# Kernel optimization log

Measured on AMD Instinct MI355X. Metric: run time of the kernel, lower is better.

The kernel has to match this reference:

```python
import jax, jax.numpy as jnp
import numpy as np

ORDER = 25
L = ORDER + 1
K = 64
B = 262144
N_ITER = 8
WEIGHT_FLOOR = 1e-05
VAR_FLOOR = 1e-06
LOG_PI = L * float(np.log(2.0 * np.pi))  # (order+1)*log(2*pi)


def setup_inputs() -> dict:
    key = jax.random.key(0)
    k1, k2 = jax.random.split(key)
    x = jax.random.normal(k1, (B, L), dtype=jnp.float32)
    mu0 = jax.random.normal(k2, (K, L), dtype=jnp.float32)      # torch.randn(K, L)
    w0 = jnp.ones((K,), dtype=jnp.float32)                      # normalized to 1/K in reference
    sigma0 = jnp.ones((K, L), dtype=jnp.float32)                # diagonal of eye(L)
    return {"x": x, "w0": w0, "mu0": mu0, "sigma0": sigma0}


def _em_step(x, w, mu, sig):
    # ---- E-step (diag covariance path of the torch module) ----
    log_det = jnp.sum(jnp.log(sig), axis=-1)                    # [K]
    prec = 1.0 / sig                                            # [K,L]
    # mahala[b,k] = sum_l (x[b,l]-mu[k,l])^2 * prec[k,l]
    # expanded quadratic form to avoid materializing [B,K,L]
    mahala = ((x * x) @ prec.T
              - 2.0 * (x @ (mu * prec).T)
              + jnp.sum(mu * mu * prec, axis=-1))               # [B,K]
    numer = jnp.log(w) - 0.5 * (LOG_PI + log_det + mahala)      # [B,K]
    denom = jax.scipy.special.logsumexp(numer, axis=-1, keepdims=True)
    posterior = jnp.exp(numer - denom)                          # [B,K]
    ll = jnp.sum(denom)
    # ---- M-step (alpha == 0) ----
    z = jnp.sum(posterior, axis=0)                              # [K]
    w_new = z / B
    zinv = 1.0 / z
    # weight flooring + renormalization
    w_new = jnp.maximum(w_new, WEIGHT_FLOOR)
    sum_floor = WEIGHT_FLOOR * K
    a = (1.0 - sum_floor) / (jnp.sum(w_new) - sum_floor)
    b = WEIGHT_FLOOR * (1.0 - a)
    w_new = a * w_new + b
    px = posterior.T @ x                                        # [K,L]
    mu_new = px * zinv[:, None]
    pxx = posterior.T @ (x * x)                                 # [K,L]
    sig_new = pxx * zinv[:, None] - mu_new * mu_new
    sig_new = jnp.maximum(sig_new, VAR_FLOOR)                   # variance flooring
    return w_new, mu_new, sig_new, ll


def reference(x, w0, mu0, sigma0):
    w = w0 / jnp.sum(w0)                                        # == 1/K for ones init

    def body(carry, _):
        w, mu, sig, _ = carry
        w, mu, sig, ll = _em_step(x, w, mu, sig)
        return (w, mu, sig, ll), None

    init = (w, mu0, sigma0, jnp.zeros((), dtype=jnp.float32))
    (w, mu, sig, ll), _ = jax.lax.scan(body, init, None, length=N_ITER)
    sigma = jax.vmap(jnp.diag)(sig)                             # [K,L,L] diagonal covariances
    return w, mu, sigma, ll
```

## Files before the change

kernel.cpp:

```cpp
#include <hip/hip_runtime.h>
#include <math.h>

typedef _Float16 f16x8 __attribute__((ext_vector_type(8)));
typedef float f32x16 __attribute__((ext_vector_type(16)));
typedef unsigned int uint4v __attribute__((ext_vector_type(4)));

namespace {
constexpr int LDIM = 26;
constexpr int KDIM = 64;
constexpr int NSAMP = 262144;
constexpr int NITER = 8;
constexpr float WFLOOR = 1e-5f;
constexpr float VFLOOR = 1e-6f;
constexpr float LOG2PI_TERM = 47.784803726642976f;
constexpr float L2E = 1.44269504088896340736f;
constexpr float LN2 = 0.69314718055994530942f;

constexpr int ACC_STRIDE = 53;
constexpr int ACC_N = KDIM * ACC_STRIDE + 1;
constexpr int NCOPIES = 8;
constexpr int WROW = 36;
constexpr int NBLK = 2048;
constexpr int PART_STRIDE = 3408;
}

__device__ float g_partial[NBLK * PART_STRIDE];
__device__ float g_accum[NCOPIES * ACC_N];
__device__ float g_w[KDIM];
__device__ float g_mu[KDIM * LDIM];
__device__ float g_sig[KDIM * LDIM];
__device__ float g_ll[1];
__device__ __align__(16) unsigned g_coef[KDIM * WROW];

__device__ __forceinline__ unsigned pkrtz(float a, float b) {
  return __builtin_bit_cast(unsigned, __builtin_amdgcn_cvt_pkrtz(a, b));
}
__device__ __forceinline__ f16x8 ld8h(const unsigned* p) {
  uint4v v = *(const uint4v*)p;
  return __builtin_bit_cast(f16x8, v);
}
__device__ __forceinline__ f32x16 mfma16(f16x8 a, f16x8 b, f32x16 c) {
  return __builtin_amdgcn_mfma_f32_32x32x16_f16(a, b, c, 0, 0, 0);
}
__device__ __forceinline__ void gload16(const void* g, void* l) {
  __builtin_amdgcn_global_load_lds(
      (const __attribute__((address_space(1))) unsigned*)g,
      (__attribute__((address_space(3))) unsigned*)l, 16, 0, 0);
}

__device__ void pack_row(int k, float w, const float* mu, const float* sg, unsigned* wp) {
  float A[LDIM], Bv[LDIM];
  float logdet = 0.f, q = 0.f;
#pragma unroll
  for (int l = 0; l < LDIM; ++l) {
    float pr = 1.0f / sg[l];
    logdet += __logf(sg[l]);
    A[l] = -0.5f * pr;
    Bv[l] = mu[l] * pr;
    q = __builtin_fmaf(mu[l] * mu[l], pr, q);
  }
  float C = __logf(w) - 0.5f * (LOG2PI_TERM + logdet + q);
  float Chi = (float)__builtin_amdgcn_cvt_pkrtz(C, 0.0f)[0];
  float Clo = C - Chi;
  unsigned* row = wp + k * WROW;
#define CF(f) ((f) < 26 ? A[(f)] : (f) < 52 ? Bv[(f) - 26] : (f) == 52 ? C : (f) == 53 ? Clo : 0.0f)
#pragma unroll
  for (int D = 0; D < 32; ++D) row[D] = pkrtz(CF(2 * D), CF(2 * D + 1));
#undef CF
#pragma unroll
  for (int D = 32; D < 36; ++D) row[D] = 0u;
}

__global__ void prep_coef(const float* __restrict__ w0, const float* __restrict__ mu0,
                          const float* __restrict__ sig0) {
  const int k = threadIdx.x;
  float wv = w0[k];
  float s = wv;
#pragma unroll
  for (int d = 1; d < 64; d <<= 1) s += __shfl_xor(s, d, 64);
  float w = wv / s;
  float mu[LDIM], sg[LDIM];
#pragma unroll
  for (int l = 0; l < LDIM; ++l) {
    mu[l] = mu0[k * LDIM + l];
    sg[l] = sig0[k * LDIM + l];
  }
  pack_row(k, w, mu, sg, g_coef);
}

__global__ __launch_bounds__(64, 2) void em_mfma(const float* __restrict__ x) {
  __shared__ __align__(16) unsigned char xtbuf[2][2048];
  __shared__ __align__(16) unsigned char ptbuf[2][2048];
  __shared__ __align__(16) float stage[2][32 * LDIM];

  const int lane = threadIdx.x & 63;
  const int sl = lane & 31;
  const int h = lane >> 5;

  unsigned short* PT0s = (unsigned short*)&ptbuf[0][0];
  unsigned short* PT1s = (unsigned short*)&ptbuf[1][0];
  const unsigned* PT0d = (const unsigned*)&ptbuf[0][0];
  const unsigned* PT1d = (const unsigned*)&ptbuf[1][0];

  f32x16 aX0 = {0,0,0,0,0,0,0,0,0,0,0,0,0,0,0,0};
  f32x16 aX1 = {0,0,0,0,0,0,0,0,0,0,0,0,0,0,0,0};
  f32x16 aQ0 = {0,0,0,0,0,0,0,0,0,0,0,0,0,0,0,0};
  f32x16 aQ1 = {0,0,0,0,0,0,0,0,0,0,0,0,0,0,0,0};
  float llacc = 0.f;

  const int sbase = blockIdx.x * 128;
  const int rowbase0 = sl * WROW;
  const int rowbase1 = (32 + sl) * WROW;

  f16x8 ca00 = ld8h(g_coef + rowbase0 + 0 + 4 * h);
  f16x8 ca01 = ld8h(g_coef + rowbase0 + 8 + 4 * h);
  f16x8 ca02 = ld8h(g_coef + rowbase0 + 16 + 4 * h);
  f16x8 ca03 = ld8h(g_coef + rowbase0 + 24 + 4 * h);
  f16x8 ca10 = ld8h(g_coef + rowbase1 + 0 + 4 * h);
  f16x8 ca11 = ld8h(g_coef + rowbase1 + 8 + 4 * h);
  f16x8 ca12 = ld8h(g_coef + rowbase1 + 16 + 4 * h);
  f16x8 ca13 = ld8h(g_coef + rowbase1 + 24 + 4 * h);

  auto stage_tile = [&](int tt) {
    const uint4v* tb = (const uint4v*)(x + (size_t)(sbase + 32 * tt) * LDIM);
    char* db = (char*)&stage[tt & 1][0];
    gload16(tb + lane, db + (size_t)lane * 16);
    gload16(tb + 64 + lane, db + 1024 + (size_t)lane * 16);
    gload16(tb + 128 + lane, db + 2048 + (size_t)lane * 16);
    if (lane < 16) gload16(tb + 192 + lane, db + 3072 + (size_t)lane * 16);
  };

  stage_tile(0);

#pragma unroll
  for (int t = 0; t < 4; ++t) {
    asm volatile("s_waitcnt vmcnt(0)" ::: "memory");

    unsigned xhu[13], squ[13];
    {
      const float2* srow = (const float2*)&stage[t & 1][sl * LDIM];
#pragma unroll
      for (int j = 0; j < 13; ++j) {
        float2 v = srow[j];
        xhu[j] = pkrtz(v.x, v.y);
        squ[j] = pkrtz(v.x * v.x, v.y * v.y);
      }
    }

    if (t < 3) stage_tile(t + 1);

    unsigned short* XTs = (unsigned short*)&xtbuf[0][0];
    unsigned short* SQs = (unsigned short*)&xtbuf[1][0];
    if (h == 0) {
#pragma unroll
      for (int c = 0; c < LDIM; ++c) {
        unsigned xvv = (c & 1) ? (xhu[c >> 1] >> 16) : (xhu[c >> 1] & 0xffffu);
        unsigned svv = (c & 1) ? (squ[c >> 1] >> 16) : (squ[c >> 1] & 0xffffu);
        const int idx = (c * 32 + sl) ^ ((c & 7) << 3);
        XTs[idx] = (unsigned short)xvv;
        SQs[idx] = (unsigned short)svv;
      }
      const int idx26 = (26 * 32 + sl) ^ ((26 & 7) << 3);
      XTs[idx26] = (unsigned short)0x3C00;
      SQs[idx26] = (unsigned short)0;
    }

    f32x16 e0 = {0,0,0,0,0,0,0,0,0,0,0,0,0,0,0,0};
    f32x16 e1 = {0,0,0,0,0,0,0,0,0,0,0,0,0,0,0,0};
    {
      uint4v b0 = {h ? squ[4] : squ[0], h ? squ[5] : squ[1],
                   h ? squ[6] : squ[2], h ? squ[7] : squ[3]};
      uint4v b1 = {h ? squ[12] : squ[8], h ? xhu[0] : squ[9],
                   h ? xhu[1] : squ[10], h ? xhu[2] : squ[11]};
      uint4v b2 = {h ? xhu[7] : xhu[3], h ? xhu[8] : xhu[4],
                   h ? xhu[9] : xhu[5], h ? xhu[10] : xhu[6]};
      uint4v b3 = {h ? 0u : xhu[11], h ? 0u : xhu[12],
                   h ? 0u : 0x3C003C00u, 0u};
      f16x8 fb0 = __builtin_bit_cast(f16x8, b0);
      f16x8 fb1 = __builtin_bit_cast(f16x8, b1);
      f16x8 fb2 = __builtin_bit_cast(f16x8, b2);
      f16x8 fb3 = __builtin_bit_cast(f16x8, b3);
      e0 = mfma16(ca00, fb0, e0);
      e1 = mfma16(ca10, fb0, e1);
      e0 = mfma16(ca01, fb1, e0);
      e1 = mfma16(ca11, fb1, e1);
      e0 = mfma16(ca02, fb2, e0);
      e1 = mfma16(ca12, fb2, e1);
      e0 = mfma16(ca03, fb3, e0);
      e1 = mfma16(ca13, fb3, e1);
    }

    float m8[8];
#pragma unroll
    for (int r = 0; r < 8; ++r)
      m8[r] = fmaxf(fmaxf(e0[r], e0[r + 8]), fmaxf(e1[r], e1[r + 8]));
#pragma unroll
    for (int d = 4; d > 0; d >>= 1)
#pragma unroll
      for (int r = 0; r < d; ++r) m8[r] = fmaxf(m8[r], m8[r + d]);
    const float M = fmaxf(m8[0], __shfl_xor(m8[0], 32));
    const float mL = M * L2E;
#pragma unroll
    for (int r = 0; r < 16; ++r) {
      e0[r] = __builtin_amdgcn_exp2f(__builtin_fmaf(e0[r], L2E, -mL));
      e1[r] = __builtin_amdgcn_exp2f(__builtin_fmaf(e1[r], L2E, -mL));
    }
    float s8[8];
#pragma unroll
    for (int r = 0; r < 8; ++r)
      s8[r] = (e0[r] + e0[r + 8]) + (e1[r] + e1[r + 8]);
#pragma unroll
    for (int d = 4; d > 0; d >>= 1)
#pragma unroll
      for (int r = 0; r < d; ++r) s8[r] += s8[r + d];
    const float SS = s8[0] + __shfl_xor(s8[0], 32);
    const float scale = __builtin_amdgcn_rcpf(SS);
    llacc += M + __builtin_amdgcn_logf(SS) * LN2;

#pragma unroll
    for (int r = 0; r < 16; ++r) {
      const int row = (r & 3) + 8 * (r >> 2) + 4 * h;
      const int idx = (row * 32 + sl) ^ ((row & 7) << 3);
      _Float16 p0 = (_Float16)(e0[r] * scale);
      _Float16 p1 = (_Float16)(e1[r] * scale);
      PT0s[idx] = __builtin_bit_cast(unsigned short, p0);
      PT1s[idx] = __builtin_bit_cast(unsigned short, p1);
    }

    const unsigned* XTd = (const unsigned*)XTs;
    const unsigned* SQd = (const unsigned*)SQs;
#pragma unroll
    for (int ks = 0; ks < 2; ++ks) {
      const int off = 8 * ks + 4 * h;
      const int swz = (sl & 7) << 2;
      f16x8 a0 = ld8h(&PT0d[(sl * 16 + off) ^ swz]);
      f16x8 a1 = ld8h(&PT1d[(sl * 16 + off) ^ swz]);
      f16x8 bx = ld8h(&XTd[(sl * 16 + off) ^ swz]);
      f16x8 bq = ld8h(&SQd[(sl * 16 + off) ^ swz]);
      aX0 = mfma16(a0, bx, aX0);
      aQ0 = mfma16(a0, bq, aQ0);
      aX1 = mfma16(a1, bx, aX1);
      aQ1 = mfma16(a1, bq, aQ1);
    }
  }

  float* pb = g_partial + (size_t)blockIdx.x * PART_STRIDE;
#pragma unroll
  for (int r = 0; r < 16; ++r) {
    const int row = (r & 3) + 8 * (r >> 2) + 4 * h;
    if (sl < 26) {
      pb[row * ACC_STRIDE + 1 + sl] = aX0[r];
      pb[row * ACC_STRIDE + 27 + sl] = aQ0[r];
      pb[(row + 32) * ACC_STRIDE + 1 + sl] = aX1[r];
      pb[(row + 32) * ACC_STRIDE + 27 + sl] = aQ1[r];
    } else if (sl == 26) {
      pb[row * ACC_STRIDE] = aX0[r];
      pb[(row + 32) * ACC_STRIDE] = aX1[r];
    }
  }
  float llw = llacc * 0.5f;
#pragma unroll
  for (int d = 1; d < 64; d <<= 1) llw += __shfl_xor(llw, d, 64);
  if (lane == 0) pb[KDIM * ACC_STRIDE] = llw;
}

__global__ void reduce_partials() {
  const int i = blockIdx.x * 256 + threadIdx.x;
  if (i >= ACC_N) return;
  const int cy = blockIdx.y;
  const float* p = g_partial + (size_t)cy * 256 * PART_STRIDE + i;
  float s = 0.f;
#pragma unroll 8
  for (int j = 0; j < 256; ++j) s += p[(size_t)j * PART_STRIDE];
  g_accum[cy * ACC_N + i] = s;
}

__global__ void finalize_k() {
  const int k = threadIdx.x;
  float vals[ACC_STRIDE];
#pragma unroll
  for (int j = 0; j < ACC_STRIDE; ++j) vals[j] = 0.f;
  float llsum = 0.f;
  for (int cp = 0; cp < NCOPIES; ++cp) {
    const float* a = g_accum + cp * ACC_N;
#pragma unroll
    for (int j = 0; j < ACC_STRIDE; ++j) vals[j] += a[k * ACC_STRIDE + j];
    llsum += a[KDIM * ACC_STRIDE];
  }
  float z = vals[0];
  float wn = z * (1.0f / NSAMP);
  float wf = fmaxf(wn, WFLOOR);
  float S = wf;
#pragma unroll
  for (int d = 1; d < 64; d <<= 1) S += __shfl_xor(S, d, 64);
  const float sf = WFLOOR * KDIM;
  float a = (1.0f - sf) / (S - sf);
  float b = WFLOOR * (1.0f - a);
  float w = a * wf + b;
  g_w[k] = w;
  float zinv = 1.0f / z;
  float muk[LDIM], sgk[LDIM];
#pragma unroll
  for (int l = 0; l < LDIM; ++l) {
    float m = vals[1 + l] * zinv;
    float s2 = fmaxf(__builtin_fmaf(-m, m, vals[27 + l] * zinv), VFLOOR);
    muk[l] = m;
    sgk[l] = s2;
    g_mu[k * LDIM + l] = m;
    g_sig[k * LDIM + l] = s2;
  }
  if (k == 0) g_ll[0] = llsum;
  pack_row(k, w, muk, sgk, g_coef);
}

__global__ void writeout(float* __restrict__ out) {
  const int i = blockIdx.x * 256 + threadIdx.x;
  if (i < 64) {
    out[i] = g_w[i];
  } else if (i < 64 + KDIM * LDIM) {
    out[i] = g_mu[i - 64];
  } else if (i < 64 + KDIM * LDIM + KDIM * LDIM * LDIM) {
    int t = i - (64 + KDIM * LDIM);
    int k = t / (LDIM * LDIM);
    int r = t % (LDIM * LDIM);
    int ii = r / LDIM;
    int jj = r % LDIM;
    out[i] = (ii == jj) ? g_sig[k * LDIM + ii] : 0.f;
  } else if (i == 64 + KDIM * LDIM + KDIM * LDIM * LDIM) {
    out[i] = g_ll[0];
  }
}

extern "C" void kernel_launch(void* const* d_in, const int* in_sizes, int n_in,
                              void* d_out, int out_size, void* d_ws, size_t ws_size,
                              hipStream_t stream) {
  (void)in_sizes; (void)n_in; (void)d_ws; (void)ws_size; (void)out_size;
  const float* x   = (const float*)d_in[0];
  const float* w0  = (const float*)d_in[1];
  const float* mu0 = (const float*)d_in[2];
  const float* sg0 = (const float*)d_in[3];
  float* out = (float*)d_out;

  prep_coef<<<1, 64, 0, stream>>>(w0, mu0, sg0);
  for (int it = 0; it < NITER; ++it) {
    em_mfma<<<NBLK, 64, 0, stream>>>(x);
    reduce_partials<<<dim3(14, 8), 256, 0, stream>>>();
    finalize_k<<<1, 64, 0, stream>>>();
  }
  const int nout = 64 + KDIM * LDIM + KDIM * LDIM * LDIM + 1;
  writeout<<<(nout + 255) / 256, 256, 0, stream>>>(out);
}
```

Before: 348.6 us.

## Use 4-warp blocks with LDS atomic partial reduction and fused last-block finalize

```diff
diff --git a/kernel.cpp b/kernel.cpp
--- a/kernel.cpp
+++ b/kernel.cpp
@@ -20,8 +20,9 @@
 constexpr int ACC_N = KDIM * ACC_STRIDE + 1;
 constexpr int NCOPIES = 8;
 constexpr int WROW = 36;
-constexpr int NBLK = 2048;
+constexpr int NBLK = 512;
 constexpr int PART_STRIDE = 3408;
+constexpr int RED_BLK = 14;
 }
 
 __device__ float g_partial[NBLK * PART_STRIDE];
@@ -31,6 +32,7 @@
 __device__ float g_sig[KDIM * LDIM];
 __device__ float g_ll[1];
 __device__ __align__(16) unsigned g_coef[KDIM * WROW];
+__device__ int g_ticket;
 
 __device__ __forceinline__ unsigned pkrtz(float a, float b) {
   return __builtin_bit_cast(unsigned, __builtin_amdgcn_cvt_pkrtz(a, b));
@@ -86,21 +88,24 @@
     sg[l] = sig0[k * LDIM + l];
   }
   pack_row(k, w, mu, sg, g_coef);
-}
-
-__global__ __launch_bounds__(64, 2) void em_mfma(const float* __restrict__ x) {
-  __shared__ __align__(16) unsigned char xtbuf[2][2048];
-  __shared__ __align__(16) unsigned char ptbuf[2][2048];
-  __shared__ __align__(16) float stage[2][32 * LDIM];
-
-  const int lane = threadIdx.x & 63;
+  if (k == 0) g_ticket = 0;
+}
+
+__global__ __launch_bounds__(256, 2) void em_mfma(const float* __restrict__ x) {
+  __shared__ __align__(16) unsigned char xtbuf[4][2][2048];
+  __shared__ __align__(16) unsigned char ptbuf[4][2][2048];
+  __shared__ __align__(16) float stage[4][2][32 * LDIM];
+
+  const int tid = threadIdx.x;
+  const int lane = tid & 63;
+  const int warp = tid >> 6;
   const int sl = lane & 31;
   const int h = lane >> 5;
 
-  unsigned short* PT0s = (unsigned short*)&ptbuf[0][0];
-  unsigned short* PT1s = (unsigned short*)&ptbuf[1][0];
-  const unsigned* PT0d = (const unsigned*)&ptbuf[0][0];
-  const unsigned* PT1d = (const unsigned*)&ptbuf[1][0];
+  unsigned short* PT0s = (unsigned short*)&ptbuf[warp][0][0];
+  unsigned short* PT1s = (unsigned short*)&ptbuf[warp][1][0];
+  const unsigned* PT0d = (const unsigned*)&ptbuf[warp][0][0];
+  const unsigned* PT1d = (const unsigned*)&ptbuf[warp][1][0];
 
   f32x16 aX0 = {0,0,0,0,0,0,0,0,0,0,0,0,0,0,0,0};
   f32x16 aX1 = {0,0,0,0,0,0,0,0,0,0,0,0,0,0,0,0};
@@ -108,7 +113,7 @@
   f32x16 aQ1 = {0,0,0,0,0,0,0,0,0,0,0,0,0,0,0,0};
   float llacc = 0.f;
 
-  const int sbase = blockIdx.x * 128;
+  const int sbase = blockIdx.x * 512 + warp * 128;
   const int rowbase0 = sl * WROW;
   const int rowbase1 = (32 + sl) * WROW;
 
@@ -123,7 +128,7 @@
 
   auto stage_tile = [&](int tt) {
     const uint4v* tb = (const uint4v*)(x + (size_t)(sbase + 32 * tt) * LDIM);
-    char* db = (char*)&stage[tt & 1][0];
+    char* db = (char*)&stage[warp][tt & 1][0];
     gload16(tb + lane, db + (size_t)lane * 16);
     gload16(tb + 64 + lane, db + 1024 + (size_t)lane * 16);
     gload16(tb + 128 + lane, db + 2048 + (size_t)lane * 16);
@@ -138,7 +143,7 @@
 
     unsigned xhu[13], squ[13];
     {
-      const float2* srow = (const float2*)&stage[t & 1][sl * LDIM];
+      const float2* srow = (const float2*)&stage[warp][t & 1][sl * LDIM];
 #pragma unroll
       for (int j = 0; j < 13; ++j) {
         float2 v = srow[j];
@@ -149,8 +154,8 @@
 
     if (t < 3) stage_tile(t + 1);
 
-    unsigned short* XTs = (unsigned short*)&xtbuf[0][0];
-    unsigned short* SQs = (unsigned short*)&xtbuf[1][0];
+    unsigned short* XTs = (unsigned short*)&xtbuf[warp][0][0];
+    unsigned short* SQs = (unsigned short*)&xtbuf[warp][1][0];
     if (h == 0) {
 #pragma unroll
       for (int c = 0; c < LDIM; ++c) {
@@ -244,39 +249,52 @@
     }
   }
 
-  float* pb = g_partial + (size_t)blockIdx.x * PART_STRIDE;
+  __syncthreads();
+  float* red = (float*)&xtbuf[0][0][0];
+  for (int i = tid; i < ACC_N; i += 256) red[i] = 0.f;
+  __syncthreads();
 #pragma unroll
   for (int r = 0; r < 16; ++r) {
     const int row = (r & 3) + 8 * (r >> 2) + 4 * h;
     if (sl < 26) {
-      pb[row * ACC_STRIDE + 1 + sl] = aX0[r];
-      pb[row * ACC_STRIDE + 27 + sl] = aQ0[r];
-      pb[(row + 32) * ACC_STRIDE + 1 + sl] = aX1[r];
-      pb[(row + 32) * ACC_STRIDE + 27 + sl] = aQ1[r];
+      atomicAdd(&red[row * ACC_STRIDE + 1 + sl], aX0[r]);
+      atomicAdd(&red[row * ACC_STRIDE + 27 + sl], aQ0[r]);
+      atomicAdd(&red[(row + 32) * ACC_STRIDE + 1 + sl], aX1[r]);
+      atomicAdd(&red[(row + 32) * ACC_STRIDE + 27 + sl], aQ1[r]);
     } else if (sl == 26) {
-      pb[row * ACC_STRIDE] = aX0[r];
-      pb[(row + 32) * ACC_STRIDE] = aX1[r];
+      atomicAdd(&red[row * ACC_STRIDE], aX0[r]);
+      atomicAdd(&red[(row + 32) * ACC_STRIDE], aX1[r]);
     }
   }
   float llw = llacc * 0.5f;
 #pragma unroll
   for (int d = 1; d < 64; d <<= 1) llw += __shfl_xor(llw, d, 64);
-  if (lane == 0) pb[KDIM * ACC_STRIDE] = llw;
-}
-
-__global__ void reduce_partials() {
+  if (lane == 0) atomicAdd(&red[KDIM * ACC_STRIDE], llw);
+  __syncthreads();
+  float* pb = g_partial + (size_t)blockIdx.x * PART_STRIDE;
+  for (int i = tid; i < ACC_N; i += 256) pb[i] = red[i];
+}
+
+__global__ void reduce_finalize() {
   const int i = blockIdx.x * 256 + threadIdx.x;
-  if (i >= ACC_N) return;
   const int cy = blockIdx.y;
-  const float* p = g_partial + (size_t)cy * 256 * PART_STRIDE + i;
-  float s = 0.f;
+  if (i < ACC_N) {
+    const float* p = g_partial + (size_t)cy * 64 * PART_STRIDE + i;
+    float s = 0.f;
 #pragma unroll 8
-  for (int j = 0; j < 256; ++j) s += p[(size_t)j * PART_STRIDE];
-  g_accum[cy * ACC_N + i] = s;
-}
-
-__global__ void finalize_k() {
+    for (int j = 0; j < 64; ++j) s += p[(size_t)j * PART_STRIDE];
+    g_accum[cy * ACC_N + i] = s;
+  }
+  __threadfence();
+  __shared__ int elect;
+  if (threadIdx.x == 0)
+    elect = (atomicAdd(&g_ticket, 1) == RED_BLK * NCOPIES - 1) ? 1 : 0;
+  __syncthreads();
+  if (elect == 0) return;
+  __threadfence();
+  if (threadIdx.x == 0) g_ticket = 0;
   const int k = threadIdx.x;
+  if (k >= 64) return;
   float vals[ACC_STRIDE];
 #pragma unroll
   for (int j = 0; j < ACC_STRIDE; ++j) vals[j] = 0.f;
@@ -343,9 +361,8 @@
 
   prep_coef<<<1, 64, 0, stream>>>(w0, mu0, sg0);
   for (int it = 0; it < NITER; ++it) {
-    em_mfma<<<NBLK, 64, 0, stream>>>(x);
-    reduce_partials<<<dim3(14, 8), 256, 0, stream>>>();
-    finalize_k<<<1, 64, 0, stream>>>();
+    em_mfma<<<NBLK, 256, 0, stream>>>(x);
+    reduce_finalize<<<dim3(RED_BLK, NCOPIES), 256, 0, stream>>>();
   }
   const int nout = 64 + KDIM * LDIM + KDIM * LDIM * LDIM + 1;
   writeout<<<(nout + 255) / 256, 256, 0, stream>>>(out);
```

New measurement: 597.0 us. 71.2% more time.

## Use two-wave blocks with in-block LDS reduction to halve global partials

Applied to the files above, without the earlier changes.

```diff
diff --git a/kernel.cpp b/kernel.cpp
--- a/kernel.cpp
+++ b/kernel.cpp
@@ -20,7 +20,7 @@
 constexpr int ACC_N = KDIM * ACC_STRIDE + 1;
 constexpr int NCOPIES = 8;
 constexpr int WROW = 36;
-constexpr int NBLK = 2048;
+constexpr int NBLK = 1024;
 constexpr int PART_STRIDE = 3408;
 }
 
@@ -88,19 +88,24 @@
   pack_row(k, w, mu, sg, g_coef);
 }
 
-__global__ __launch_bounds__(64, 2) void em_mfma(const float* __restrict__ x) {
-  __shared__ __align__(16) unsigned char xtbuf[2][2048];
-  __shared__ __align__(16) unsigned char ptbuf[2][2048];
-  __shared__ __align__(16) float stage[2][32 * LDIM];
-
-  const int lane = threadIdx.x & 63;
+__global__ __launch_bounds__(128, 2) void em_mfma(const float* __restrict__ x) {
+  __shared__ __align__(16) unsigned char pool[16384];
+  __shared__ __align__(16) float stage[2][2][32 * LDIM];
+
+  const int tid = threadIdx.x;
+  const int lane = tid & 63;
+  const int warp = tid >> 6;
   const int sl = lane & 31;
   const int h = lane >> 5;
 
-  unsigned short* PT0s = (unsigned short*)&ptbuf[0][0];
-  unsigned short* PT1s = (unsigned short*)&ptbuf[1][0];
-  const unsigned* PT0d = (const unsigned*)&ptbuf[0][0];
-  const unsigned* PT1d = (const unsigned*)&ptbuf[1][0];
+  unsigned short* XTs = (unsigned short*)&pool[warp * 4096];
+  unsigned short* SQs = (unsigned short*)&pool[warp * 4096 + 2048];
+  unsigned short* PT0s = (unsigned short*)&pool[8192 + warp * 4096];
+  unsigned short* PT1s = (unsigned short*)&pool[8192 + warp * 4096 + 2048];
+  const unsigned* XTd = (const unsigned*)XTs;
+  const unsigned* SQd = (const unsigned*)SQs;
+  const unsigned* PT0d = (const unsigned*)PT0s;
+  const unsigned* PT1d = (const unsigned*)PT1s;
 
   f32x16 aX0 = {0,0,0,0,0,0,0,0,0,0,0,0,0,0,0,0};
   f32x16 aX1 = {0,0,0,0,0,0,0,0,0,0,0,0,0,0,0,0};
@@ -108,7 +113,7 @@
   f32x16 aQ1 = {0,0,0,0,0,0,0,0,0,0,0,0,0,0,0,0};
   float llacc = 0.f;
 
-  const int sbase = blockIdx.x * 128;
+  const int sbase = blockIdx.x * 256 + warp * 128;
   const int rowbase0 = sl * WROW;
   const int rowbase1 = (32 + sl) * WROW;
 
@@ -123,7 +128,7 @@
 
   auto stage_tile = [&](int tt) {
     const uint4v* tb = (const uint4v*)(x + (size_t)(sbase + 32 * tt) * LDIM);
-    char* db = (char*)&stage[tt & 1][0];
+    char* db = (char*)&stage[warp][tt & 1][0];
     gload16(tb + lane, db + (size_t)lane * 16);
     gload16(tb + 64 + lane, db + 1024 + (size_t)lane * 16);
     gload16(tb + 128 + lane, db + 2048 + (size_t)lane * 16);
@@ -138,7 +143,7 @@
 
     unsigned xhu[13], squ[13];
     {
-      const float2* srow = (const float2*)&stage[t & 1][sl * LDIM];
+      const float2* srow = (const float2*)&stage[warp][t & 1][sl * LDIM];
 #pragma unroll
       for (int j = 0; j < 13; ++j) {
         float2 v = srow[j];
@@ -149,20 +154,15 @@
 
     if (t < 3) stage_tile(t + 1);
 
-    unsigned short* XTs = (unsigned short*)&xtbuf[0][0];
-    unsigned short* SQs = (unsigned short*)&xtbuf[1][0];
-    if (h == 0) {
+    {
+      unsigned short* Ts = h ? SQs : XTs;
 #pragma unroll
       for (int c = 0; c < LDIM; ++c) {
-        unsigned xvv = (c & 1) ? (xhu[c >> 1] >> 16) : (xhu[c >> 1] & 0xffffu);
-        unsigned svv = (c & 1) ? (squ[c >> 1] >> 16) : (squ[c >> 1] & 0xffffu);
-        const int idx = (c * 32 + sl) ^ ((c & 7) << 3);
-        XTs[idx] = (unsigned short)xvv;
-        SQs[idx] = (unsigned short)svv;
+        unsigned src = h ? squ[c >> 1] : xhu[c >> 1];
+        unsigned v = (c & 1) ? (src >> 16) : (src & 0xffffu);
+        Ts[(c * 32 + sl) ^ ((c & 7) << 3)] = (unsigned short)v;
       }
-      const int idx26 = (26 * 32 + sl) ^ ((26 & 7) << 3);
-      XTs[idx26] = (unsigned short)0x3C00;
-      SQs[idx26] = (unsigned short)0;
+      Ts[(26 * 32 + sl) ^ ((26 & 7) << 3)] = h ? (unsigned short)0 : (unsigned short)0x3C00;
     }
 
     f32x16 e0 = {0,0,0,0,0,0,0,0,0,0,0,0,0,0,0,0};
@@ -227,8 +227,6 @@
       PT1s[idx] = __builtin_bit_cast(unsigned short, p1);
     }
 
-    const unsigned* XTd = (const unsigned*)XTs;
-    const unsigned* SQd = (const unsigned*)SQs;
 #pragma unroll
     for (int ks = 0; ks < 2; ++ks) {
       const int off = 8 * ks + 4 * h;
@@ -244,34 +242,55 @@
     }
   }
 
-  float* pb = g_partial + (size_t)blockIdx.x * PART_STRIDE;
-#pragma unroll
-  for (int r = 0; r < 16; ++r) {
-    const int row = (r & 3) + 8 * (r >> 2) + 4 * h;
-    if (sl < 26) {
-      pb[row * ACC_STRIDE + 1 + sl] = aX0[r];
-      pb[row * ACC_STRIDE + 27 + sl] = aQ0[r];
-      pb[(row + 32) * ACC_STRIDE + 1 + sl] = aX1[r];
-      pb[(row + 32) * ACC_STRIDE + 27 + sl] = aQ1[r];
-    } else if (sl == 26) {
-      pb[row * ACC_STRIDE] = aX0[r];
-      pb[(row + 32) * ACC_STRIDE] = aX1[r];
-    }
-  }
+  __syncthreads();
+  float* red = (float*)&pool[0];
   float llw = llacc * 0.5f;
 #pragma unroll
   for (int d = 1; d < 64; d <<= 1) llw += __shfl_xor(llw, d, 64);
-  if (lane == 0) pb[KDIM * ACC_STRIDE] = llw;
+  if (warp == 0) {
+#pragma unroll
+    for (int r = 0; r < 16; ++r) {
+      const int row = (r & 3) + 8 * (r >> 2) + 4 * h;
+      if (sl < 26) {
+        red[row * ACC_STRIDE + 1 + sl] = aX0[r];
+        red[row * ACC_STRIDE + 27 + sl] = aQ0[r];
+        red[(row + 32) * ACC_STRIDE + 1 + sl] = aX1[r];
+        red[(row + 32) * ACC_STRIDE + 27 + sl] = aQ1[r];
+      } else if (sl == 26) {
+        red[row * ACC_STRIDE] = aX0[r];
+        red[(row + 32) * ACC_STRIDE] = aX1[r];
+      }
+    }
+    if (lane == 0) red[KDIM * ACC_STRIDE] = llw;
+  }
+  __syncthreads();
+  if (warp == 1) {
+    float* pb = g_partial + (size_t)blockIdx.x * PART_STRIDE;
+#pragma unroll
+    for (int r = 0; r < 16; ++r) {
+      const int row = (r & 3) + 8 * (r >> 2) + 4 * h;
+      if (sl < 26) {
+        pb[row * ACC_STRIDE + 1 + sl] = red[row * ACC_STRIDE + 1 + sl] + aX0[r];
+        pb[row * ACC_STRIDE + 27 + sl] = red[row * ACC_STRIDE + 27 + sl] + aQ0[r];
+        pb[(row + 32) * ACC_STRIDE + 1 + sl] = red[(row + 32) * ACC_STRIDE + 1 + sl] + aX1[r];
+        pb[(row + 32) * ACC_STRIDE + 27 + sl] = red[(row + 32) * ACC_STRIDE + 27 + sl] + aQ1[r];
+      } else if (sl == 26) {
+        pb[row * ACC_STRIDE] = red[row * ACC_STRIDE] + aX0[r];
+        pb[(row + 32) * ACC_STRIDE] = red[(row + 32) * ACC_STRIDE] + aX1[r];
+      }
+    }
+    if (lane == 0) pb[KDIM * ACC_STRIDE] = red[KDIM * ACC_STRIDE] + llw;
+  }
 }
 
 __global__ void reduce_partials() {
   const int i = blockIdx.x * 256 + threadIdx.x;
   if (i >= ACC_N) return;
   const int cy = blockIdx.y;
-  const float* p = g_partial + (size_t)cy * 256 * PART_STRIDE + i;
+  const float* p = g_partial + (size_t)cy * 128 * PART_STRIDE + i;
   float s = 0.f;
 #pragma unroll 8
-  for (int j = 0; j < 256; ++j) s += p[(size_t)j * PART_STRIDE];
+  for (int j = 0; j < 128; ++j) s += p[(size_t)j * PART_STRIDE];
   g_accum[cy * ACC_N + i] = s;
 }
 
@@ -343,7 +362,7 @@
 
   prep_coef<<<1, 64, 0, stream>>>(w0, mu0, sg0);
   for (int it = 0; it < NITER; ++it) {
-    em_mfma<<<NBLK, 64, 0, stream>>>(x);
+    em_mfma<<<NBLK, 128, 0, stream>>>(x);
     reduce_partials<<<dim3(14, 8), 256, 0, stream>>>();
     finalize_k<<<1, 64, 0, stream>>>();
   }
```

New measurement: 301.5 us. 1.16x faster.
